# Optimization experiments

Measured on AMD Instinct MI355X. Metric: run time of the kernel, lower is better.

## Reference

```python
import jax, jax.numpy as jnp
import numpy as np

N_ENT, N_REL, N_EDGE = 50000, 500, 500000
L_LAYERS, HEADS, DIM = 2, 2, 64
POW_ITER, ALPHA, LN_EPS = 3, 0.15, 1e-5


def setup_inputs() -> dict:
    key = jax.random.key(0)
    ks = jax.random.split(key, 13)
    s = 1.0 / np.sqrt(DIM)
    return {
        "entity_embed": jax.random.normal(ks[0], (N_ENT, DIM), jnp.float32) * 0.05,
        "relation_embed": jax.random.normal(ks[1], (N_REL, DIM), jnp.float32) * 0.05,
        "edge_index": jax.random.randint(ks[2], (2, N_EDGE), 0, N_ENT, jnp.int32),
        "edge_type": jax.random.randint(ks[3], (N_EDGE,), 0, N_REL, jnp.int32),
        "ln_gamma": jnp.ones((L_LAYERS, DIM), jnp.float32),
        "ln_beta": jnp.zeros((L_LAYERS, DIM), jnp.float32),
        "W_h": jax.random.normal(ks[4], (L_LAYERS, DIM, HEADS * DIM), jnp.float32) * s,
        "W_t": jax.random.normal(ks[5], (L_LAYERS, DIM, HEADS * DIM), jnp.float32) * s,
        "W_r": jax.random.normal(ks[6], (L_LAYERS, DIM, HEADS * DIM), jnp.float32) * s,
        "att_h": jax.random.normal(ks[7], (L_LAYERS, HEADS, DIM), jnp.float32) * s,
        "att_t": jax.random.normal(ks[8], (L_LAYERS, HEADS, DIM), jnp.float32) * s,
        "att_r": jax.random.normal(ks[9], (L_LAYERS, HEADS, DIM), jnp.float32) * s,
        "W_o": jax.random.normal(ks[10], (L_LAYERS, HEADS * DIM, DIM), jnp.float32) * s,
    }


def _layernorm(x, g, b):
    mu = jnp.mean(x, axis=-1, keepdims=True)
    var = jnp.mean(jnp.square(x - mu), axis=-1, keepdims=True)
    return (x - mu) * jax.lax.rsqrt(var + LN_EPS) * g + b


def _node_scores(h, W, att):
    # h: [M, D], W: [D, H*D], att: [H, D] -> [M, H]
    t = jnp.tanh((h @ W).reshape(h.shape[0], HEADS, DIM))
    return jnp.einsum("mhd,hd->mh", t, att)


def _segment_softmax(scores, seg, num_segments):
    # scores: [E, H] grouped by seg (head node ids)
    m = jax.ops.segment_max(scores, seg, num_segments=num_segments)
    e = jnp.exp(scores - m[seg])
    z = jax.ops.segment_sum(e, seg, num_segments=num_segments)
    return e / z[seg]


def reference(entity_embed, relation_embed, edge_index, edge_type,
              ln_gamma, ln_beta, W_h, W_t, W_r, att_h, att_t, att_r, W_o):
    src, dst = edge_index[0], edge_index[1]  # head_ids, tail_ids
    n = entity_embed.shape[0]
    ent = entity_embed
    for l in range(L_LAYERS):
        x = ent
        h = _layernorm(x, ln_gamma[l], ln_beta[l])  # eval mode: dropout off
        # per-node / per-relation attention score contributions, then gather per edge
        s_h = _node_scores(h, W_h[l], att_h[l])               # [N, H]
        s_t = _node_scores(h, W_t[l], att_t[l])               # [N, H]
        s_r = _node_scores(relation_embed, W_r[l], att_r[l])  # [R, H]
        scores = jax.nn.leaky_relu(s_h[src] + s_t[dst] + s_r[edge_type])  # [E, H]
        w = _segment_softmax(scores, src, n)                  # segment softmax by head_ids
        A = (1.0 - ALPHA) * w                                 # [E, H]
        # PPR power iteration (all heads vectorized), Z0 = Z_init = h
        Z = jnp.broadcast_to(h[:, None, :], (n, HEADS, DIM))
        aZ0 = ALPHA * h[:, None, :]
        for _ in range(POW_ITER):
            msg = A[:, :, None] * Z[dst]                      # [E, H, D]
            Z = jax.ops.segment_sum(msg, src, num_segments=n) + aZ0
        conv = Z.reshape(n, HEADS * DIM) @ W_o[l]             # [N, D]
        ent = conv + x  # residual; MLP output in source is discarded (typo bug)
    return ent
```

## Files before the change

kernel.cpp:

```cpp
#include <hip/hip_runtime.h>

#define N_ENT 50000
#define N_REL 500
#define N_EDGE 500000
#define HEADS 2
#define DIM 64
#define POW_ITER 3
#define ALPHA 0.15f
#define LN_EPS 1e-5f
#define NBLK 49

typedef unsigned uv4 __attribute__((ext_vector_type(4)));
typedef short bf16x8 __attribute__((ext_vector_type(8)));
typedef float f32x4 __attribute__((ext_vector_type(4)));

static __device__ __forceinline__ unsigned bf16_rne(float f) {
  unsigned u = __float_as_uint(f);
  return (u + 0x7FFFu + ((u >> 16) & 1u)) >> 16;
}

__global__ void deg_kernel(const int* __restrict__ src, int* __restrict__ deg) {
  int e = blockIdx.x * blockDim.x + threadIdx.x;
  if (e >= N_EDGE) return;
  atomicAdd(&deg[src[e]], 1);
}

__global__ __launch_bounds__(1024) void scan1_kernel(const int* __restrict__ deg,
                                                     int* __restrict__ exc,
                                                     int* __restrict__ bsum) {
  __shared__ int tmp[1024];
  int tid = threadIdx.x;
  int i = blockIdx.x * 1024 + tid;
  int v = (i < N_ENT) ? deg[i] : 0;
  tmp[tid] = v;
  __syncthreads();
  for (int off = 1; off < 1024; off <<= 1) {
    int t = (tid >= off) ? tmp[tid - off] : 0;
    __syncthreads();
    tmp[tid] += t;
    __syncthreads();
  }
  if (i < N_ENT) exc[i] = tmp[tid] - v;
  if (tid == 1023) bsum[blockIdx.x] = tmp[1023];
}

__global__ void scan2_kernel(const int* __restrict__ bsum, int* __restrict__ boff) {
  int t = threadIdx.x;
  int v = (t < NBLK) ? bsum[t] : 0;
  int incl = v;
#pragma unroll
  for (int off = 1; off < 64; off <<= 1) {
    int u = __shfl_up(incl, off);
    if (t >= off) incl += u;
  }
  if (t < NBLK) boff[t] = incl - v;
  if (t == NBLK - 1) boff[NBLK] = incl;
}

__global__ __launch_bounds__(1024) void scan3_kernel(const int* __restrict__ exc,
                                                     const int* __restrict__ boff,
                                                     int* __restrict__ rowptr) {
  int i = blockIdx.x * 1024 + threadIdx.x;
  if (i < N_ENT) rowptr[i] = exc[i] + boff[i >> 10];
  if (i == N_ENT) rowptr[N_ENT] = boff[NBLK];
}

__global__ void scatter_kernel(const int* __restrict__ src, const int* __restrict__ dst,
                               const int* __restrict__ et, int* __restrict__ cursor,
                               int* __restrict__ csr_src, int* __restrict__ csr_dst,
                               int* __restrict__ csr_et) {
  int e = blockIdx.x * blockDim.x + threadIdx.x;
  if (e >= N_EDGE) return;
  int s = src[e];
  int p = atomicAdd(&cursor[s], 1);
  csr_src[p] = s;
  csr_dst[p] = dst[e];
  csr_et[p] = et[e];
}

__global__ void ln_kernel(const float* __restrict__ x, const float* __restrict__ g,
                          const float* __restrict__ b, float* __restrict__ h,
                          unsigned short* __restrict__ h_bf) {
  int wid = (blockIdx.x * blockDim.x + threadIdx.x) >> 6;
  int lane = threadIdx.x & 63;
  if (wid >= N_ENT) return;
  float v = x[wid * 64 + lane];
  float s = v;
#pragma unroll
  for (int off = 32; off; off >>= 1) s += __shfl_xor(s, off);
  float mu = s * (1.0f / 64.0f);
  float d = v - mu;
  float s2 = d * d;
#pragma unroll
  for (int off = 32; off; off >>= 1) s2 += __shfl_xor(s2, off);
  float rs = rsqrtf(s2 * (1.0f / 64.0f) + LN_EPS);
  float hv = d * rs * g[lane] + b[lane];
  h[wid * 64 + lane] = hv;
  h_bf[wid * 64 + lane] = (unsigned short)bf16_rne(hv);
}

__global__ __launch_bounds__(256) void scores2_mfma_kernel(
    const unsigned short* __restrict__ h_bf, const float* __restrict__ Wh,
    const float* __restrict__ Wt, const float* __restrict__ ah,
    const float* __restrict__ at, float* __restrict__ s_h, float* __restrict__ s_t) {
  __shared__ uv4 Bfrag[2][8][2][64];
  int tid = threadIdx.x;
  for (int idx = tid; idx < 2 * 8 * 2 * 64; idx += 256) {
    int l = idx & 63;
    int ks = (idx >> 6) & 1;
    int ct = (idx >> 7) & 7;
    int mat = idx >> 10;
    const float* W = mat ? Wt : Wh;
    int col = ct * 16 + (l & 15);
    int kbase = ks * 32 + (l >> 4) * 8;
    unsigned v[8];
#pragma unroll
    for (int j = 0; j < 8; ++j) v[j] = bf16_rne(W[(kbase + j) * 128 + col]);
    uv4 q;
    q.x = v[0] | (v[1] << 16);
    q.y = v[2] | (v[3] << 16);
    q.z = v[4] | (v[5] << 16);
    q.w = v[6] | (v[7] << 16);
    Bfrag[mat][ct][ks][l] = q;
  }
  __syncthreads();
  int lane = tid & 63;
  int l15 = lane & 15;
  int kg = lane >> 4;
  float attv[2][8];
#pragma unroll
  for (int ct = 0; ct < 8; ++ct) {
    attv[0][ct] = ah[ct * 16 + l15];
    attv[1][ct] = at[ct * 16 + l15];
  }
  int wave = (blockIdx.x * 256 + tid) >> 6;
  int nwaves = (gridDim.x * 256) >> 6;
  const int NT = N_ENT / 16;
  for (int t = wave; t < NT; t += nwaves) {
    int n0 = t * 16;
    const unsigned short* zrow = h_bf + (size_t)(n0 + l15) * 64 + kg * 8;
    bf16x8 A0 = *(const bf16x8*)(zrow);
    bf16x8 A1 = *(const bf16x8*)(zrow + 32);
    float ph[2][2][4];
#pragma unroll
    for (int m2 = 0; m2 < 2; ++m2)
#pragma unroll
      for (int hd = 0; hd < 2; ++hd)
#pragma unroll
        for (int r = 0; r < 4; ++r) ph[m2][hd][r] = 0.f;
#pragma unroll
    for (int mat = 0; mat < 2; ++mat) {
#pragma unroll
      for (int ct = 0; ct < 8; ++ct) {
        f32x4 a = {0.f, 0.f, 0.f, 0.f};
        a = __builtin_amdgcn_mfma_f32_16x16x32_bf16(A0, *(bf16x8*)&Bfrag[mat][ct][0][lane], a, 0, 0, 0);
        a = __builtin_amdgcn_mfma_f32_16x16x32_bf16(A1, *(bf16x8*)&Bfrag[mat][ct][1][lane], a, 0, 0, 0);
        int hd = ct >> 2;
        float av = attv[mat][ct];
#pragma unroll
        for (int r = 0; r < 4; ++r) ph[mat][hd][r] += tanhf(a[r]) * av;
      }
    }
#pragma unroll
    for (int mat = 0; mat < 2; ++mat)
#pragma unroll
      for (int hd = 0; hd < 2; ++hd)
#pragma unroll
        for (int r = 0; r < 4; ++r) {
          float v = ph[mat][hd][r];
          v += __shfl_xor(v, 1);
          v += __shfl_xor(v, 2);
          v += __shfl_xor(v, 4);
          v += __shfl_xor(v, 8);
          ph[mat][hd][r] = v;
        }
    if (l15 == 0) {
#pragma unroll
      for (int r = 0; r < 4; ++r) {
        int row = n0 + kg * 4 + r;
        ((float2*)s_h)[row] = make_float2(ph[0][0][r], ph[0][1][r]);
        ((float2*)s_t)[row] = make_float2(ph[1][0][r], ph[1][1][r]);
      }
    }
  }
}

__global__ __launch_bounds__(256) void scores_kernel(
    const float* __restrict__ x, const float* __restrict__ W,
    const float* __restrict__ att, float* __restrict__ s_out, int M) {
  __shared__ float4 WP4[32][64];
  for (int i = threadIdx.x; i < 32 * 64; i += 256) {
    int k2 = i >> 6, j = i & 63;
    WP4[k2][j] = make_float4(W[(2 * k2) * 128 + j], W[(2 * k2) * 128 + j + 64],
                             W[(2 * k2 + 1) * 128 + j], W[(2 * k2 + 1) * 128 + j + 64]);
  }
  __syncthreads();
  int lane = threadIdx.x & 63;
  float a0v = att[lane], a1v = att[lane + 64];
  int gw = (blockIdx.x * 256 + threadIdx.x) >> 6;
  int nw = (gridDim.x * 256) >> 6;
  for (int n0 = 2 * gw; n0 < M; n0 += 2 * nw) {
    int nu = __builtin_amdgcn_readfirstlane(n0);
    const float* xr0 = x + nu * 64;
    const float* xr1 = x + (nu + 1) * 64;
    float a00 = 0.f, a01 = 0.f, a10 = 0.f, a11 = 0.f;
#pragma unroll 8
    for (int k2 = 0; k2 < 32; ++k2) {
      float4 wv = WP4[k2][lane];
      float xa0 = xr0[2 * k2], xa1 = xr0[2 * k2 + 1];
      float xb0 = xr1[2 * k2], xb1 = xr1[2 * k2 + 1];
      a00 += xa0 * wv.x + xa1 * wv.z;
      a01 += xa0 * wv.y + xa1 * wv.w;
      a10 += xb0 * wv.x + xb1 * wv.z;
      a11 += xb0 * wv.y + xb1 * wv.w;
    }
    float t00 = tanhf(a00) * a0v, t01 = tanhf(a01) * a1v;
    float t10 = tanhf(a10) * a0v, t11 = tanhf(a11) * a1v;
#pragma unroll
    for (int off = 32; off; off >>= 1) {
      t00 += __shfl_xor(t00, off);
      t01 += __shfl_xor(t01, off);
      t10 += __shfl_xor(t10, off);
      t11 += __shfl_xor(t11, off);
    }
    if (lane == 0) {
      ((float2*)s_out)[nu] = make_float2(t00, t01);
      ((float2*)s_out)[nu + 1] = make_float2(t10, t11);
    }
  }
}

__global__ void edge_w_kernel(const int* __restrict__ csr_src, const int* __restrict__ csr_dst,
                              const int* __restrict__ csr_et, const float* __restrict__ s_h,
                              const float* __restrict__ s_t, const float* __restrict__ s_r,
                              float* __restrict__ csr_w) {
  int p = blockIdx.x * blockDim.x + threadIdx.x;
  if (p >= N_EDGE) return;
  int s = csr_src[p], d = csr_dst[p], r = csr_et[p];
  float2 a = ((const float2*)s_h)[s];
  float2 b = ((const float2*)s_t)[d];
  float2 c = ((const float2*)s_r)[r];
  float sc0 = a.x + b.x + c.x;
  float sc1 = a.y + b.y + c.y;
  sc0 = (sc0 >= 0.f) ? sc0 : 0.01f * sc0;
  sc1 = (sc1 >= 0.f) ? sc1 : 0.01f * sc1;
  ((float2*)csr_w)[p] = make_float2(expf(sc0), expf(sc1));
}

__global__ __launch_bounds__(256) void cinv_kernel(const int* __restrict__ rowptr,
                                                   const float* __restrict__ csr_w,
                                                   float* __restrict__ cinv) {
  int n = (blockIdx.x * 256 + threadIdx.x) >> 6;
  int lane = threadIdx.x & 63;
  if (n >= N_ENT) return;
  int p0 = rowptr[n], p1 = rowptr[n + 1];
  float z0 = 0.f, z1 = 0.f;
  for (int p = p0 + lane; p < p1; p += 64) {
    float2 w2 = ((const float2*)csr_w)[p];
    z0 += w2.x;
    z1 += w2.y;
  }
#pragma unroll
  for (int off = 32; off; off >>= 1) {
    z0 += __shfl_xor(z0, off);
    z1 += __shfl_xor(z1, off);
  }
  if (lane == 0) {
    float c0 = (p1 > p0) ? (1.0f - ALPHA) / z0 : 0.f;
    float c1 = (p1 > p0) ? (1.0f - ALPHA) / z1 : 0.f;
    ((float2*)cinv)[n] = make_float2(c0, c1);
  }
}

template <int IN_H>
__global__ __launch_bounds__(256) void spmm_kernel(
    const int* __restrict__ rowptr, const int* __restrict__ csr_dst,
    const float* __restrict__ csr_w, const float* __restrict__ cinv,
    const float* __restrict__ h, const unsigned short* __restrict__ Zin_b,
    unsigned short* __restrict__ Zout_b) {
  int lane = threadIdx.x & 63;
  int slot = lane >> 4;
  int l16 = lane & 15;
  int hh = l16 >> 3;
  int hoff = 8 * (l16 & 7);
  int gw = (blockIdx.x * 256 + threadIdx.x) >> 6;
  int nw = (gridDim.x * 256) >> 6;
  for (int n = gw; n < N_ENT; n += nw) {
    int p0 = rowptr[n], p1 = rowptr[n + 1];
    float acc[8];
#pragma unroll
    for (int j = 0; j < 8; ++j) acc[j] = 0.f;
    for (int p = p0 + slot; p < p1; p += 4) {
      int d = csr_dst[p];
      float2 w2 = ((const float2*)csr_w)[p];
      float a = hh ? w2.y : w2.x;
      uv4 q;
      if (IN_H) {
        q = *(const uv4*)(Zin_b + d * 64 + hoff);
      } else {
        q = *(const uv4*)(Zin_b + d * 128 + 8 * l16);
      }
      acc[0] += a * __uint_as_float(q.x << 16);
      acc[1] += a * __uint_as_float(q.x & 0xFFFF0000u);
      acc[2] += a * __uint_as_float(q.y << 16);
      acc[3] += a * __uint_as_float(q.y & 0xFFFF0000u);
      acc[4] += a * __uint_as_float(q.z << 16);
      acc[5] += a * __uint_as_float(q.z & 0xFFFF0000u);
      acc[6] += a * __uint_as_float(q.w << 16);
      acc[7] += a * __uint_as_float(q.w & 0xFFFF0000u);
    }
#pragma unroll
    for (int j = 0; j < 8; ++j) {
      acc[j] += __shfl_xor(acc[j], 16);
      acc[j] += __shfl_xor(acc[j], 32);
    }
    if (slot == 0) {
      float c = cinv[n * 2 + hh];
      const float* hp = h + n * 64 + hoff;
      float o[8];
#pragma unroll
      for (int j = 0; j < 8; ++j) o[j] = ALPHA * hp[j] + c * acc[j];
      uv4 qo;
      qo.x = bf16_rne(o[0]) | (bf16_rne(o[1]) << 16);
      qo.y = bf16_rne(o[2]) | (bf16_rne(o[3]) << 16);
      qo.z = bf16_rne(o[4]) | (bf16_rne(o[5]) << 16);
      qo.w = bf16_rne(o[6]) | (bf16_rne(o[7]) << 16);
      *(uv4*)(Zout_b + n * 128 + 8 * l16) = qo;
    }
  }
}

__global__ __launch_bounds__(256) void out_mfma_kernel(
    const unsigned short* __restrict__ Zb, const float* __restrict__ Wo,
    const float* __restrict__ x, float* __restrict__ out) {
  __shared__ uv4 Bfrag[4][4][64];
  int tid = threadIdx.x;
  for (int idx = tid; idx < 4 * 4 * 64; idx += 256) {
    int ct = idx >> 8, ks = (idx >> 6) & 3, l = idx & 63;
    int col = ct * 16 + (l & 15);
    int kbase = ks * 32 + (l >> 4) * 8;
    unsigned v[8];
#pragma unroll
    for (int j = 0; j < 8; ++j) v[j] = bf16_rne(Wo[(kbase + j) * 64 + col]);
    uv4 q;
    q.x = v[0] | (v[1] << 16);
    q.y = v[2] | (v[3] << 16);
    q.z = v[4] | (v[5] << 16);
    q.w = v[6] | (v[7] << 16);
    Bfrag[ct][ks][l] = q;
  }
  __syncthreads();
  int lane = tid & 63;
  bf16x8 B[4][4];
#pragma unroll
  for (int ct = 0; ct < 4; ++ct)
#pragma unroll
    for (int ks = 0; ks < 4; ++ks) B[ct][ks] = *(bf16x8*)&Bfrag[ct][ks][lane];

  int m = lane & 15;
  int kg = lane >> 4;
  int wave = (blockIdx.x * 256 + tid) >> 6;
  int nwaves = (gridDim.x * 256) >> 6;
  const int NT = N_ENT / 16;
  for (int t = wave; t < NT; t += nwaves) {
    int n0 = t * 16;
    const unsigned short* zrow = Zb + (size_t)(n0 + m) * 128 + kg * 8;
    bf16x8 A0 = *(const bf16x8*)(zrow);
    bf16x8 A1 = *(const bf16x8*)(zrow + 32);
    bf16x8 A2 = *(const bf16x8*)(zrow + 64);
    bf16x8 A3 = *(const bf16x8*)(zrow + 96);
    f32x4 acc[4];
#pragma unroll
    for (int ct = 0; ct < 4; ++ct) {
      f32x4 a = {0.f, 0.f, 0.f, 0.f};
      a = __builtin_amdgcn_mfma_f32_16x16x32_bf16(A0, B[ct][0], a, 0, 0, 0);
      a = __builtin_amdgcn_mfma_f32_16x16x32_bf16(A1, B[ct][1], a, 0, 0, 0);
      a = __builtin_amdgcn_mfma_f32_16x16x32_bf16(A2, B[ct][2], a, 0, 0, 0);
      a = __builtin_amdgcn_mfma_f32_16x16x32_bf16(A3, B[ct][3], a, 0, 0, 0);
      acc[ct] = a;
    }
#pragma unroll
    for (int r = 0; r < 4; ++r) {
      int rr = n0 + kg * 4 + r;
#pragma unroll
      for (int ct = 0; ct < 4; ++ct) {
        int cc = ct * 16 + (lane & 15);
        out[rr * 64 + cc] = acc[ct][r] + x[rr * 64 + cc];
      }
    }
  }
}

extern "C" void kernel_launch(void* const* d_in, const int* in_sizes, int n_in,
                              void* d_out, int out_size, void* d_ws, size_t ws_size,
                              hipStream_t stream) {
  const float* ent0 = (const float*)d_in[0];
  const float* rel  = (const float*)d_in[1];
  const int* eidx   = (const int*)d_in[2];
  const int* src    = eidx;
  const int* dst    = eidx + N_EDGE;
  const int* et     = (const int*)d_in[3];
  const float* gam  = (const float*)d_in[4];
  const float* bet  = (const float*)d_in[5];
  const float* W_h  = (const float*)d_in[6];
  const float* W_t  = (const float*)d_in[7];
  const float* W_r  = (const float*)d_in[8];
  const float* att_h = (const float*)d_in[9];
  const float* att_t = (const float*)d_in[10];
  const float* att_r = (const float*)d_in[11];
  const float* W_o  = (const float*)d_in[12];
  float* outp = (float*)d_out;

  char* w = (char*)d_ws;
  auto alloc = [&](size_t bytes) {
    char* p = w;
    w += (bytes + 255) & ~(size_t)255;
    return p;
  };
  float* ent1   = (float*)alloc((size_t)N_ENT * 64 * 4);
  float* h      = (float*)alloc((size_t)N_ENT * 64 * 4);
  unsigned short* h_bf = (unsigned short*)alloc((size_t)N_ENT * 64 * 2);
  float* s_h    = (float*)alloc((size_t)N_ENT * 2 * 4);
  float* s_t    = (float*)alloc((size_t)N_ENT * 2 * 4);
  float* s_r    = (float*)alloc((size_t)N_REL * 2 * 4);
  float* cinv   = (float*)alloc((size_t)N_ENT * 2 * 4);
  float* csr_w  = (float*)alloc((size_t)N_EDGE * 2 * 4);
  unsigned short* Zb0 = (unsigned short*)alloc((size_t)N_ENT * 128 * 2);
  unsigned short* Zb1 = (unsigned short*)alloc((size_t)N_ENT * 128 * 2);
  int* deg      = (int*)alloc((size_t)N_ENT * 4);
  int* exc      = (int*)alloc((size_t)N_ENT * 4);
  int* bsum     = (int*)alloc((size_t)NBLK * 4);
  int* boff     = (int*)alloc((size_t)(NBLK + 1) * 4);
  int* rowptr   = (int*)alloc((size_t)(N_ENT + 1) * 4);
  int* cursor   = (int*)alloc((size_t)N_ENT * 4);
  int* csr_src  = (int*)alloc((size_t)N_EDGE * 4);
  int* csr_dst  = (int*)alloc((size_t)N_EDGE * 4);
  int* csr_et   = (int*)alloc((size_t)N_EDGE * 4);

  const int EB = (N_EDGE + 255) / 256;

  hipMemsetAsync(deg, 0, (size_t)N_ENT * 4, stream);
  deg_kernel<<<EB, 256, 0, stream>>>(src, deg);
  scan1_kernel<<<NBLK, 1024, 0, stream>>>(deg, exc, bsum);
  scan2_kernel<<<1, 64, 0, stream>>>(bsum, boff);
  scan3_kernel<<<NBLK, 1024, 0, stream>>>(exc, boff, rowptr);
  hipMemcpyAsync(cursor, rowptr, (size_t)N_ENT * 4, hipMemcpyDeviceToDevice, stream);
  scatter_kernel<<<EB, 256, 0, stream>>>(src, dst, et, cursor, csr_src, csr_dst, csr_et);

  for (int l = 0; l < 2; ++l) {
    const float* x = (l == 0) ? ent0 : ent1;
    float* y = (l == 0) ? ent1 : outp;

    ln_kernel<<<(N_ENT + 3) / 4, 256, 0, stream>>>(x, gam + l * 64, bet + l * 64, h, h_bf);
    scores2_mfma_kernel<<<784, 256, 0, stream>>>(h_bf, W_h + l * 8192, W_t + l * 8192,
                                                 att_h + l * 128, att_t + l * 128, s_h, s_t);
    scores_kernel<<<8, 256, 0, stream>>>(rel, W_r + l * 8192, att_r + l * 128, s_r, N_REL);

    edge_w_kernel<<<EB, 256, 0, stream>>>(csr_src, csr_dst, csr_et, s_h, s_t, s_r, csr_w);
    cinv_kernel<<<(N_ENT * 64 + 255) / 256, 256, 0, stream>>>(rowptr, csr_w, cinv);

    spmm_kernel<1><<<2048, 256, 0, stream>>>(rowptr, csr_dst, csr_w, cinv, h, h_bf, Zb0);
    spmm_kernel<0><<<2048, 256, 0, stream>>>(rowptr, csr_dst, csr_w, cinv, h, Zb0, Zb1);
    spmm_kernel<0><<<2048, 256, 0, stream>>>(rowptr, csr_dst, csr_w, cinv, h, Zb1, Zb0);

    out_mfma_kernel<<<512, 256, 0, stream>>>(Zb0, W_o + l * 8192, x, y);
  }
}
```

Measured before the change: 426.8 us.

## Fuse edge weight and normalizer kernels, pack dst/etype, retune grid sizes

Packs each CSR edge's destination node and relation type into a single 32-bit word, dropping the separate src/dst/etype arrays. Merges the per-edge exp-score kernel into the per-node normalizer kernel, so edges are handled per row and the head score is loaded once per node. Also shrinks the launch grids of the node-score and output MFMA kernels. This relies on node ids fitting in 16 bits and on those kernels looping over work when given fewer blocks.

```diff
diff --git a/kernel.cpp b/kernel.cpp
--- a/kernel.cpp
+++ b/kernel.cpp
@@ -67,15 +67,12 @@
 
 __global__ void scatter_kernel(const int* __restrict__ src, const int* __restrict__ dst,
                                const int* __restrict__ et, int* __restrict__ cursor,
-                               int* __restrict__ csr_src, int* __restrict__ csr_dst,
-                               int* __restrict__ csr_et) {
+                               unsigned* __restrict__ csr_de) {
   int e = blockIdx.x * blockDim.x + threadIdx.x;
   if (e >= N_EDGE) return;
   int s = src[e];
   int p = atomicAdd(&cursor[s], 1);
-  csr_src[p] = s;
-  csr_dst[p] = dst[e];
-  csr_et[p] = et[e];
+  csr_de[p] = (unsigned)dst[e] | ((unsigned)et[e] << 16);
 }
 
 __global__ void ln_kernel(const float* __restrict__ x, const float* __restrict__ g,
@@ -230,35 +227,30 @@
   }
 }
 
-__global__ void edge_w_kernel(const int* __restrict__ csr_src, const int* __restrict__ csr_dst,
-                              const int* __restrict__ csr_et, const float* __restrict__ s_h,
-                              const float* __restrict__ s_t, const float* __restrict__ s_r,
-                              float* __restrict__ csr_w) {
-  int p = blockIdx.x * blockDim.x + threadIdx.x;
-  if (p >= N_EDGE) return;
-  int s = csr_src[p], d = csr_dst[p], r = csr_et[p];
-  float2 a = ((const float2*)s_h)[s];
-  float2 b = ((const float2*)s_t)[d];
-  float2 c = ((const float2*)s_r)[r];
-  float sc0 = a.x + b.x + c.x;
-  float sc1 = a.y + b.y + c.y;
-  sc0 = (sc0 >= 0.f) ? sc0 : 0.01f * sc0;
-  sc1 = (sc1 >= 0.f) ? sc1 : 0.01f * sc1;
-  ((float2*)csr_w)[p] = make_float2(expf(sc0), expf(sc1));
-}
-
-__global__ __launch_bounds__(256) void cinv_kernel(const int* __restrict__ rowptr,
-                                                   const float* __restrict__ csr_w,
-                                                   float* __restrict__ cinv) {
+__global__ __launch_bounds__(256) void edge_cinv_kernel(
+    const int* __restrict__ rowptr, const unsigned* __restrict__ csr_de,
+    const float* __restrict__ s_h, const float* __restrict__ s_t,
+    const float* __restrict__ s_r, float* __restrict__ csr_w, float* __restrict__ cinv) {
   int n = (blockIdx.x * 256 + threadIdx.x) >> 6;
   int lane = threadIdx.x & 63;
   if (n >= N_ENT) return;
   int p0 = rowptr[n], p1 = rowptr[n + 1];
+  float2 sh = ((const float2*)s_h)[n];
   float z0 = 0.f, z1 = 0.f;
   for (int p = p0 + lane; p < p1; p += 64) {
-    float2 w2 = ((const float2*)csr_w)[p];
-    z0 += w2.x;
-    z1 += w2.y;
+    unsigned de = csr_de[p];
+    int d = de & 0xFFFF;
+    int r = de >> 16;
+    float2 st = ((const float2*)s_t)[d];
+    float2 sr = ((const float2*)s_r)[r];
+    float sc0 = sh.x + st.x + sr.x;
+    float sc1 = sh.y + st.y + sr.y;
+    sc0 = (sc0 >= 0.f) ? sc0 : 0.01f * sc0;
+    sc1 = (sc1 >= 0.f) ? sc1 : 0.01f * sc1;
+    float w0 = expf(sc0), w1 = expf(sc1);
+    ((float2*)csr_w)[p] = make_float2(w0, w1);
+    z0 += w0;
+    z1 += w1;
   }
 #pragma unroll
   for (int off = 32; off; off >>= 1) {
@@ -274,7 +266,7 @@
 
 template <int IN_H>
 __global__ __launch_bounds__(256) void spmm_kernel(
-    const int* __restrict__ rowptr, const int* __restrict__ csr_dst,
+    const int* __restrict__ rowptr, const unsigned* __restrict__ csr_de,
     const float* __restrict__ csr_w, const float* __restrict__ cinv,
     const float* __restrict__ h, const unsigned short* __restrict__ Zin_b,
     unsigned short* __restrict__ Zout_b) {
@@ -291,7 +283,7 @@
 #pragma unroll
     for (int j = 0; j < 8; ++j) acc[j] = 0.f;
     for (int p = p0 + slot; p < p1; p += 4) {
-      int d = csr_dst[p];
+      int d = csr_de[p] & 0xFFFF;
       float2 w2 = ((const float2*)csr_w)[p];
       float a = hh ? w2.y : w2.x;
       uv4 q;
@@ -433,9 +425,7 @@
   int* boff     = (int*)alloc((size_t)(NBLK + 1) * 4);
   int* rowptr   = (int*)alloc((size_t)(N_ENT + 1) * 4);
   int* cursor   = (int*)alloc((size_t)N_ENT * 4);
-  int* csr_src  = (int*)alloc((size_t)N_EDGE * 4);
-  int* csr_dst  = (int*)alloc((size_t)N_EDGE * 4);
-  int* csr_et   = (int*)alloc((size_t)N_EDGE * 4);
+  unsigned* csr_de = (unsigned*)alloc((size_t)N_EDGE * 4);
 
   const int EB = (N_EDGE + 255) / 256;
 
@@ -445,24 +435,24 @@
   scan2_kernel<<<1, 64, 0, stream>>>(bsum, boff);
   scan3_kernel<<<NBLK, 1024, 0, stream>>>(exc, boff, rowptr);
   hipMemcpyAsync(cursor, rowptr, (size_t)N_ENT * 4, hipMemcpyDeviceToDevice, stream);
-  scatter_kernel<<<EB, 256, 0, stream>>>(src, dst, et, cursor, csr_src, csr_dst, csr_et);
+  scatter_kernel<<<EB, 256, 0, stream>>>(src, dst, et, cursor, csr_de);
 
   for (int l = 0; l < 2; ++l) {
     const float* x = (l == 0) ? ent0 : ent1;
     float* y = (l == 0) ? ent1 : outp;
 
     ln_kernel<<<(N_ENT + 3) / 4, 256, 0, stream>>>(x, gam + l * 64, bet + l * 64, h, h_bf);
-    scores2_mfma_kernel<<<784, 256, 0, stream>>>(h_bf, W_h + l * 8192, W_t + l * 8192,
+    scores2_mfma_kernel<<<192, 256, 0, stream>>>(h_bf, W_h + l * 8192, W_t + l * 8192,
                                                  att_h + l * 128, att_t + l * 128, s_h, s_t);
     scores_kernel<<<8, 256, 0, stream>>>(rel, W_r + l * 8192, att_r + l * 128, s_r, N_REL);
 
-    edge_w_kernel<<<EB, 256, 0, stream>>>(csr_src, csr_dst, csr_et, s_h, s_t, s_r, csr_w);
-    cinv_kernel<<<(N_ENT * 64 + 255) / 256, 256, 0, stream>>>(rowptr, csr_w, cinv);
-
-    spmm_kernel<1><<<2048, 256, 0, stream>>>(rowptr, csr_dst, csr_w, cinv, h, h_bf, Zb0);
-    spmm_kernel<0><<<2048, 256, 0, stream>>>(rowptr, csr_dst, csr_w, cinv, h, Zb0, Zb1);
-    spmm_kernel<0><<<2048, 256, 0, stream>>>(rowptr, csr_dst, csr_w, cinv, h, Zb1, Zb0);
-
-    out_mfma_kernel<<<512, 256, 0, stream>>>(Zb0, W_o + l * 8192, x, y);
-  }
-}
+    edge_cinv_kernel<<<(N_ENT + 3) / 4, 256, 0, stream>>>(rowptr, csr_de, s_h, s_t, s_r,
+                                                          csr_w, cinv);
+
+    spmm_kernel<1><<<2048, 256, 0, stream>>>(rowptr, csr_de, csr_w, cinv, h, h_bf, Zb0);
+    spmm_kernel<0><<<2048, 256, 0, stream>>>(rowptr, csr_de, csr_w, cinv, h, Zb0, Zb1);
+    spmm_kernel<0><<<2048, 256, 0, stream>>>(rowptr, csr_de, csr_w, cinv, h, Zb1, Zb0);
+
+    out_mfma_kernel<<<160, 256, 0, stream>>>(Zb0, W_o + l * 8192, x, y);
+  }
+}
```

Result: faster. 417.8 us (-2.1%).
